# Optimization experiments

Measured on AMD Instinct MI355X. Metric: run time of the kernel, lower is better.

Reference implementation:

```python
import jax, jax.numpy as jnp
import numpy as np

B, L, D, H = 2, 2048, 1024, 16
DPH = D // H  # 64
EPS = 1e-5


def setup_inputs() -> dict:
    rng = jax.random.key(0)
    ks = jax.random.split(rng, 16)
    init = lambda k, shape: (jax.random.normal(k, shape, dtype=jnp.float32) * 0.02)
    return {
        "key": jax.random.normal(ks[0], (B, L, D), dtype=jnp.float32),
        "value": jax.random.normal(ks[1], (B, L, D), dtype=jnp.float32),
        "query": jax.random.normal(ks[2], (B, L, D), dtype=jnp.float32),
        "Wq": init(ks[3], (D, D)), "bq": jnp.zeros((D,), jnp.float32),
        "Wk": init(ks[4], (D, D)), "bk": jnp.zeros((D,), jnp.float32),
        "Wv": init(ks[5], (D, D)), "bv": jnp.zeros((D,), jnp.float32),
        "Wo": init(ks[6], (D, D)), "bo": jnp.zeros((D,), jnp.float32),
        "gamma": jnp.ones((D,), jnp.float32),
        "beta": jnp.zeros((D,), jnp.float32),
    }


def reference(key, value, query, Wq, bq, Wk, bk, Wv, bv, Wo, bo, gamma, beta):
    residual_in = query
    # torch Linear: x @ W.T + b
    k = key @ Wk.T + bk
    v = value @ Wv.T + bv
    q = query @ Wq.T + bq
    # faithful to source: flat view into (B*H, L, DPH) WITHOUT head transpose
    k = k.reshape(B * H, L, DPH)
    v = v.reshape(B * H, L, DPH)
    q = q.reshape(B * H, L, DPH)
    # faithful quirky scale: (dim_per_head // num_heads) ** -0.5
    scale = (DPH // H) ** (-0.5)
    scores = jnp.einsum("bqd,bkd->bqk", q, k) * scale  # [B*H, L, L]
    attention = jax.nn.softmax(scores, axis=2)
    context = jnp.einsum("bqk,bkd->bqd", attention, v)  # [B*H, L, DPH]
    context = context.reshape(B, L, D)
    output = context @ Wo.T + bo
    x = residual_in + output
    mean = jnp.mean(x, axis=-1, keepdims=True)
    var = jnp.var(x, axis=-1, keepdims=True)
    output = (x - mean) * jax.lax.rsqrt(var + EPS) * gamma + beta
    return (output, attention)
```

## Files before the change

### kernel.cpp

```cpp
#include <hip/hip_runtime.h>
#include <cstddef>
#include <cstdint>

#define Lseq   2048
#define Dmodel 1024
#define NGRP   32
#define MROWS  4096
#define EPS_LN 1e-5f

typedef short  s16x8 __attribute__((ext_vector_type(8)));
typedef float  f32x4 __attribute__((ext_vector_type(4)));
typedef unsigned short ushort_t;

__device__ __forceinline__ ushort_t f2bf(float f) {
    union { float f; unsigned u; } v; v.f = f;
    unsigned r = v.u + 0x7FFFu + ((v.u >> 16) & 1u);
    return (ushort_t)(r >> 16);
}

__device__ __forceinline__ unsigned cvt_pk_bf16(float lo, float hi) {
    unsigned r;
    asm("v_cvt_pk_bf16_f32 %0, %1, %2" : "=v"(r) : "v"(lo), "v"(hi));
    return r;
}

__device__ __forceinline__ void gld16(const ushort_t* g, ushort_t* lds) {
    __builtin_amdgcn_global_load_lds(
        (const __attribute__((address_space(1))) unsigned int*)(uintptr_t)g,
        (__attribute__((address_space(3))) unsigned int*)(uintptr_t)lds,
        16, 0, 0);
}

__device__ __forceinline__ int xcd_chunk32(int f) {
    return (f & 7) * 4 + ((f >> 3) & 3);
}

struct CvtArgs {
    const float* src[7];
    ushort_t*    dst[7];
    int          n8[7];
};

__global__ __launch_bounds__(256) void cvt_bf16(CvtArgs a)
{
    const int ti = blockIdx.y;
    const float* __restrict__ s = a.src[ti];
    ushort_t* __restrict__    d = a.dst[ti];
    const int n8 = a.n8[ti];
    for (int i = blockIdx.x * 256 + threadIdx.x; i < n8; i += gridDim.x * 256) {
        float4 x0 = reinterpret_cast<const float4*>(s)[i * 2];
        float4 x1 = reinterpret_cast<const float4*>(s)[i * 2 + 1];
        s16x8 o;
        o[0]=f2bf(x0.x); o[1]=f2bf(x0.y); o[2]=f2bf(x0.z); o[3]=f2bf(x0.w);
        o[4]=f2bf(x1.x); o[5]=f2bf(x1.y); o[6]=f2bf(x1.z); o[7]=f2bf(x1.w);
        reinterpret_cast<s16x8*>(d)[i] = o;
    }
}

struct QkvArgs {
    const ushort_t* A[3];
    const ushort_t* W[3];
    const float*    bias[3];
    ushort_t*       out[3];
};

__global__ __launch_bounds__(256) void gemm_qkv(QkvArgs a)
{
    __shared__ ushort_t As[128 * 64];
    __shared__ ushort_t Bs[128 * 64];
    const int z  = blockIdx.z;
    const int f  = blockIdx.x;
    const int m0 = xcd_chunk32(f) * 128;
    const int n0 = (f >> 5) * 128;

    const ushort_t* __restrict__ A = a.A[z];
    const ushort_t* __restrict__ W = a.W[z];
    const float*    __restrict__ bias = a.bias[z];
    ushort_t*       __restrict__ outv = a.out[z];

    const int t  = threadIdx.x;
    const int w  = t >> 6;
    const int l  = t & 63;
    const int lr = l & 15;
    const int lg = l >> 4;
    const int wm = w >> 1, wn = w & 1;

    const ushort_t* gA = A + (size_t)(m0 + w * 32 + (l >> 3)) * 1024 + (l & 7) * 8;
    const ushort_t* gB = W + (size_t)(n0 + w * 32 + (l >> 3)) * 1024 + (l & 7) * 8;
    ushort_t* lA = &As[(w * 32) * 64];
    ushort_t* lB = &Bs[(w * 32) * 64];

    f32x4 acc[4][4] = {};

    for (int k0 = 0; k0 < 1024; k0 += 64) {
#pragma unroll
        for (int j = 0; j < 4; ++j) {
            gld16(gA + (size_t)j * 8 * 1024 + k0, lA + j * 8 * 64);
            gld16(gB + (size_t)j * 8 * 1024 + k0, lB + j * 8 * 64);
        }
        __syncthreads();

#pragma unroll
        for (int kk = 0; kk < 2; ++kk) {
            s16x8 af[4], bf[4];
#pragma unroll
            for (int mi = 0; mi < 4; ++mi)
                af[mi] = *reinterpret_cast<const s16x8*>(&As[(wm * 64 + mi * 16 + lr) * 64 + kk * 32 + lg * 8]);
#pragma unroll
            for (int ni = 0; ni < 4; ++ni)
                bf[ni] = *reinterpret_cast<const s16x8*>(&Bs[(wn * 64 + ni * 16 + lr) * 64 + kk * 32 + lg * 8]);
#pragma unroll
            for (int mi = 0; mi < 4; ++mi)
#pragma unroll
                for (int ni = 0; ni < 4; ++ni)
                    acc[mi][ni] = __builtin_amdgcn_mfma_f32_16x16x32_bf16(af[mi], bf[ni], acc[mi][ni], 0, 0, 0);
        }
        __syncthreads();
    }

#pragma unroll
    for (int mi = 0; mi < 4; ++mi)
#pragma unroll
        for (int ni = 0; ni < 4; ++ni)
#pragma unroll
            for (int r = 0; r < 4; ++r) {
                int row = m0 + wm * 64 + mi * 16 + lg * 4 + r;
                int col = n0 + wn * 64 + ni * 16 + lr;
                outv[(size_t)row * 1024 + col] = f2bf(acc[mi][ni][r] + bias[col]);
            }
}

__global__ __launch_bounds__(256) void gemm_o(
    const ushort_t* __restrict__ A, const ushort_t* __restrict__ W,
    const float* __restrict__ bias, const float* __restrict__ resid,
    float* __restrict__ out)
{
    __shared__ ushort_t As[64 * 64];
    __shared__ ushort_t Bs[128 * 64];

    const int f  = blockIdx.x;
    const int m0 = ((f & 7) * 8 + ((f >> 3) & 7)) * 64;
    const int n0 = (f >> 6) * 128;

    const int t  = threadIdx.x;
    const int w  = t >> 6;
    const int l  = t & 63;
    const int lr = l & 15;
    const int lg = l >> 4;
    const int wm = w >> 1, wn = w & 1;

    const ushort_t* gA = A + (size_t)(m0 + w * 16 + (l >> 3)) * 1024 + (l & 7) * 8;
    const ushort_t* gB = W + (size_t)(n0 + w * 32 + (l >> 3)) * 1024 + (l & 7) * 8;
    ushort_t* lA = &As[(w * 16) * 64];
    ushort_t* lB = &Bs[(w * 32) * 64];

    f32x4 acc[2][4] = {};

    for (int k0 = 0; k0 < 1024; k0 += 64) {
#pragma unroll
        for (int j = 0; j < 2; ++j)
            gld16(gA + (size_t)j * 8 * 1024 + k0, lA + j * 8 * 64);
#pragma unroll
        for (int j = 0; j < 4; ++j)
            gld16(gB + (size_t)j * 8 * 1024 + k0, lB + j * 8 * 64);
        __syncthreads();

#pragma unroll
        for (int kk = 0; kk < 2; ++kk) {
            s16x8 af[2], bf[4];
#pragma unroll
            for (int mi = 0; mi < 2; ++mi)
                af[mi] = *reinterpret_cast<const s16x8*>(&As[(wm * 32 + mi * 16 + lr) * 64 + kk * 32 + lg * 8]);
#pragma unroll
            for (int ni = 0; ni < 4; ++ni)
                bf[ni] = *reinterpret_cast<const s16x8*>(&Bs[(wn * 64 + ni * 16 + lr) * 64 + kk * 32 + lg * 8]);
#pragma unroll
            for (int mi = 0; mi < 2; ++mi)
#pragma unroll
                for (int ni = 0; ni < 4; ++ni)
                    acc[mi][ni] = __builtin_amdgcn_mfma_f32_16x16x32_bf16(af[mi], bf[ni], acc[mi][ni], 0, 0, 0);
        }
        __syncthreads();
    }

#pragma unroll
    for (int mi = 0; mi < 2; ++mi)
#pragma unroll
        for (int ni = 0; ni < 4; ++ni)
#pragma unroll
            for (int r = 0; r < 4; ++r) {
                int row = m0 + wm * 32 + mi * 16 + lg * 4 + r;
                int col = n0 + wn * 64 + ni * 16 + lr;
                float v = acc[mi][ni][r] + bias[col] + resid[(size_t)row * 1024 + col];
                out[(size_t)row * 1024 + col] = v;
            }
}

__global__ __launch_bounds__(256) void transpose_v(
    const ushort_t* __restrict__ vb, ushort_t* __restrict__ vt)
{
    __shared__ ushort_t tile[64][72];
    const int g  = blockIdx.x;
    const int lt = blockIdx.y;
    const int t  = threadIdx.x;
#pragma unroll
    for (int it = 0; it < 2; ++it) {
        int s = t * 2 + it, row = s >> 3, sub = (s & 7) * 8;
        *reinterpret_cast<s16x8*>(&tile[row][sub]) =
            *reinterpret_cast<const s16x8*>(vb + ((size_t)(g*2048 + lt*64 + row))*64 + sub);
    }
    __syncthreads();
#pragma unroll
    for (int it = 0; it < 2; ++it) {
        int s = t * 2 + it, drow = s >> 3, sub = (s & 7) * 8;
        s16x8 o;
#pragma unroll
        for (int j = 0; j < 8; ++j) o[j] = (short)tile[sub + j][drow];
        *reinterpret_cast<s16x8*>(vt + ((size_t)(g*64 + drow))*2048 + lt*64 + sub) = o;
    }
}

__global__ __launch_bounds__(256) void attn_stats(
    const ushort_t* __restrict__ qb, const ushort_t* __restrict__ kb,
    float* __restrict__ invb)
{
    __shared__ ushort_t Ks[2][64][72];

    const int f  = blockIdx.x;
    const int g  = xcd_chunk32(f);
    const int r0 = (f >> 5) * 128;
    const int t  = threadIdx.x;
    const int w  = t >> 6;
    const int l  = t & 63;
    const int lr = l & 15;
    const int lg = l >> 4;
    const int srow0 = (t*2)   >> 3, ssub0 = ((t*2)   & 7) * 8;
    const int srow1 = (t*2+1) >> 3, ssub1 = ((t*2+1) & 7) * 8;

    s16x8 qf[2][2];
#pragma unroll
    for (int rf = 0; rf < 2; ++rf) {
        const ushort_t* qrow = qb + ((size_t)(g*2048 + r0 + w*32 + rf*16 + lr)) * 64;
        qf[rf][0] = *reinterpret_cast<const s16x8*>(qrow + lg*8);
        qf[rf][1] = *reinterpret_cast<const s16x8*>(qrow + 32 + lg*8);
    }

    *reinterpret_cast<s16x8*>(&Ks[0][srow0][ssub0]) =
        *reinterpret_cast<const s16x8*>(kb + ((size_t)(g*2048 + srow0))*64 + ssub0);
    *reinterpret_cast<s16x8*>(&Ks[0][srow1][ssub1]) =
        *reinterpret_cast<const s16x8*>(kb + ((size_t)(g*2048 + srow1))*64 + ssub1);
    __syncthreads();

    float lsum[2][4] = {};
    int cur = 0;

    for (int jc = 0; jc < 32; ++jc) {
        s16x8 nk0, nk1;
        if (jc < 31) {
            nk0 = *reinterpret_cast<const s16x8*>(kb + ((size_t)(g*2048 + (jc+1)*64 + srow0))*64 + ssub0);
            nk1 = *reinterpret_cast<const s16x8*>(kb + ((size_t)(g*2048 + (jc+1)*64 + srow1))*64 + ssub1);
        }
#pragma unroll
        for (int jf = 0; jf < 4; ++jf) {
            s16x8 b0 = *reinterpret_cast<const s16x8*>(&Ks[cur][jf*16 + lr][lg*8]);
            s16x8 b1 = *reinterpret_cast<const s16x8*>(&Ks[cur][jf*16 + lr][32 + lg*8]);
#pragma unroll
            for (int rf = 0; rf < 2; ++rf) {
                f32x4 sv = {};
                sv = __builtin_amdgcn_mfma_f32_16x16x32_bf16(qf[rf][0], b0, sv, 0, 0, 0);
                sv = __builtin_amdgcn_mfma_f32_16x16x32_bf16(qf[rf][1], b1, sv, 0, 0, 0);
#pragma unroll
                for (int r = 0; r < 4; ++r)
                    lsum[rf][r] += __expf(sv[r] * 0.5f);
            }
        }
        if (jc < 31) {
            *reinterpret_cast<s16x8*>(&Ks[cur^1][srow0][ssub0]) = nk0;
            *reinterpret_cast<s16x8*>(&Ks[cur^1][srow1][ssub1]) = nk1;
        }
        __syncthreads();
        cur ^= 1;
    }

#pragma unroll
    for (int rf = 0; rf < 2; ++rf)
#pragma unroll
        for (int r = 0; r < 4; ++r) {
            float v = lsum[rf][r];
            v += __shfl_xor(v, 1); v += __shfl_xor(v, 2);
            v += __shfl_xor(v, 4); v += __shfl_xor(v, 8);
            if (lr == 0)
                invb[(size_t)g*2048 + r0 + w*32 + rf*16 + lg*4 + r] = 1.f / v;
        }
}

__global__ __launch_bounds__(256) void attn_main(
    const ushort_t* __restrict__ qb, const ushort_t* __restrict__ kb,
    const ushort_t* __restrict__ vt, const float* __restrict__ invb,
    float* __restrict__ attn, ushort_t* __restrict__ ctxb)
{
    __shared__ ushort_t Ks[2][64][72];
    __shared__ ushort_t Vs[2][64][72];
    __shared__ ushort_t Ps[64][72];

    const int f  = blockIdx.x;
    const int g  = xcd_chunk32(f);
    const int r0 = (f >> 5) * 64;
    const int t  = threadIdx.x;
    const int w  = t >> 6;
    const int l  = t & 63;
    const int lr = l & 15;
    const int lg = l >> 4;
    const int srow0 = (t*2)   >> 3, ssub0 = ((t*2)   & 7) * 8;
    const int srow1 = (t*2+1) >> 3, ssub1 = ((t*2+1) & 7) * 8;

    s16x8 qf0, qf1;
    {
        const ushort_t* qrow = qb + ((size_t)(g*2048 + r0 + w*16 + lr)) * 64;
        qf0 = *reinterpret_cast<const s16x8*>(qrow + lg*8);
        qf1 = *reinterpret_cast<const s16x8*>(qrow + 32 + lg*8);
    }

    const float inv_s = invb[(size_t)g*2048 + r0 + w*16 + lr];
    float* arow = attn + (size_t)g*Lseq*Lseq + (size_t)(r0 + w*16 + lr)*Lseq + lg*4;

    *reinterpret_cast<s16x8*>(&Ks[0][srow0][ssub0]) =
        *reinterpret_cast<const s16x8*>(kb + ((size_t)(g*2048 + srow0))*64 + ssub0);
    *reinterpret_cast<s16x8*>(&Ks[0][srow1][ssub1]) =
        *reinterpret_cast<const s16x8*>(kb + ((size_t)(g*2048 + srow1))*64 + ssub1);
    *reinterpret_cast<s16x8*>(&Vs[0][srow0][ssub0]) =
        *reinterpret_cast<const s16x8*>(vt + ((size_t)(g*64 + srow0))*2048 + ssub0);
    *reinterpret_cast<s16x8*>(&Vs[0][srow1][ssub1]) =
        *reinterpret_cast<const s16x8*>(vt + ((size_t)(g*64 + srow1))*2048 + ssub1);
    __syncthreads();

    f32x4 ctx[4] = {};
    int cur = 0;

    for (int jc = 0; jc < 32; ++jc) {
        s16x8 nk0, nk1, nv0, nv1;
        if (jc < 31) {
            nk0 = *reinterpret_cast<const s16x8*>(kb + ((size_t)(g*2048 + (jc+1)*64 + srow0))*64 + ssub0);
            nk1 = *reinterpret_cast<const s16x8*>(kb + ((size_t)(g*2048 + (jc+1)*64 + srow1))*64 + ssub1);
            nv0 = *reinterpret_cast<const s16x8*>(vt + ((size_t)(g*64 + srow0))*2048 + (jc+1)*64 + ssub0);
            nv1 = *reinterpret_cast<const s16x8*>(vt + ((size_t)(g*64 + srow1))*2048 + (jc+1)*64 + ssub1);
        }

#pragma unroll
        for (int jf = 0; jf < 4; ++jf) {
            s16x8 a0 = *reinterpret_cast<const s16x8*>(&Ks[cur][jf*16 + lr][lg*8]);
            s16x8 a1 = *reinterpret_cast<const s16x8*>(&Ks[cur][jf*16 + lr][32 + lg*8]);
            f32x4 s = {};
            s = __builtin_amdgcn_mfma_f32_16x16x32_bf16(a0, qf0, s, 0, 0, 0);
            s = __builtin_amdgcn_mfma_f32_16x16x32_bf16(a1, qf1, s, 0, 0, 0);

            float e0 = __expf(s[0] * 0.5f);
            float e1 = __expf(s[1] * 0.5f);
            float e2 = __expf(s[2] * 0.5f);
            float e3 = __expf(s[3] * 0.5f);

            f32x4 o;
            o[0] = e0 * inv_s; o[1] = e1 * inv_s; o[2] = e2 * inv_s; o[3] = e3 * inv_s;
            *reinterpret_cast<f32x4*>(arow + jc*64 + jf*16) = o;

            unsigned p01 = cvt_pk_bf16(e0, e1);
            unsigned p23 = cvt_pk_bf16(e2, e3);
            uint2 pk; pk.x = p01; pk.y = p23;
            *reinterpret_cast<uint2*>(&Ps[w*16 + lr][jf*16 + lg*4]) = pk;
        }

#pragma unroll
        for (int kk = 0; kk < 2; ++kk) {
            s16x8 pa = *reinterpret_cast<const s16x8*>(&Ps[w*16 + lr][kk*32 + lg*8]);
#pragma unroll
            for (int ni = 0; ni < 4; ++ni) {
                s16x8 bv = *reinterpret_cast<const s16x8*>(&Vs[cur][ni*16 + lr][kk*32 + lg*8]);
                ctx[ni] = __builtin_amdgcn_mfma_f32_16x16x32_bf16(pa, bv, ctx[ni], 0, 0, 0);
            }
        }

        if (jc < 31) {
            *reinterpret_cast<s16x8*>(&Ks[cur^1][srow0][ssub0]) = nk0;
            *reinterpret_cast<s16x8*>(&Ks[cur^1][srow1][ssub1]) = nk1;
            *reinterpret_cast<s16x8*>(&Vs[cur^1][srow0][ssub0]) = nv0;
            *reinterpret_cast<s16x8*>(&Vs[cur^1][srow1][ssub1]) = nv1;
        }
        __syncthreads();
        cur ^= 1;
    }

#pragma unroll
    for (int ni = 0; ni < 4; ++ni)
#pragma unroll
        for (int r = 0; r < 4; ++r) {
            int l2 = r0 + w*16 + lg*4 + r;
            int d2 = ni*16 + lr;
            float iv = invb[(size_t)g*2048 + l2];
            ctxb[(size_t)g*Lseq*64 + (size_t)l2*64 + d2] = f2bf(ctx[ni][r] * iv);
        }
}

__global__ __launch_bounds__(256) void ln_kernel(
    float* __restrict__ x, const float* __restrict__ gamma,
    const float* __restrict__ beta, float* __restrict__ out)
{
    const int row = blockIdx.x;
    const int t   = threadIdx.x;
    const int c   = t * 4;

    float4 v = *reinterpret_cast<const float4*>(x + (size_t)row * Dmodel + c);
    float s  = v.x + v.y + v.z + v.w;
    float s2 = v.x*v.x + v.y*v.y + v.z*v.z + v.w*v.w;
    for (int off = 1; off < 64; off <<= 1) {
        s  += __shfl_xor(s, off);
        s2 += __shfl_xor(s2, off);
    }
    __shared__ float ssum[4], ssum2[4];
    int wid = t >> 6;
    if ((t & 63) == 0) { ssum[wid] = s; ssum2[wid] = s2; }
    __syncthreads();
    s  = ssum[0] + ssum[1] + ssum[2] + ssum[3];
    s2 = ssum2[0] + ssum2[1] + ssum2[2] + ssum2[3];

    float mean = s * (1.f / Dmodel);
    float var  = s2 * (1.f / Dmodel) - mean * mean;
    float rstd = rsqrtf(var + EPS_LN);

    float4 gv = *reinterpret_cast<const float4*>(gamma + c);
    float4 bv = *reinterpret_cast<const float4*>(beta + c);
    float4 o;
    o.x = (v.x - mean) * rstd * gv.x + bv.x;
    o.y = (v.y - mean) * rstd * gv.y + bv.y;
    o.z = (v.z - mean) * rstd * gv.z + bv.z;
    o.w = (v.w - mean) * rstd * gv.w + bv.w;
    *reinterpret_cast<float4*>(out + (size_t)row * Dmodel + c) = o;
}

extern "C" void kernel_launch(void* const* d_in, const int* in_sizes, int n_in,
                              void* d_out, int out_size, void* d_ws, size_t ws_size,
                              hipStream_t stream)
{
    const float* key   = (const float*)d_in[0];
    const float* value = (const float*)d_in[1];
    const float* query = (const float*)d_in[2];
    const float* Wq    = (const float*)d_in[3];
    const float* bq    = (const float*)d_in[4];
    const float* Wk    = (const float*)d_in[5];
    const float* bk    = (const float*)d_in[6];
    const float* Wv    = (const float*)d_in[7];
    const float* bv    = (const float*)d_in[8];
    const float* Wo    = (const float*)d_in[9];
    const float* bo    = (const float*)d_in[10];
    const float* gamma = (const float*)d_in[11];
    const float* beta  = (const float*)d_in[12];

    float* out  = (float*)d_out;
    float* attn = out + (size_t)MROWS * Dmodel;

    const size_t M1 = 1024 * 1024;
    ushort_t* ws   = (ushort_t*)d_ws;
    ushort_t* qb   = ws;
    ushort_t* kb   = ws + 4  * M1;
    ushort_t* vb   = ws + 8  * M1;
    ushort_t* vt   = ws + 12 * M1;
    ushort_t* qx   = ws + 16 * M1;
    ushort_t* kx   = ws + 20 * M1;
    ushort_t* vx   = ws + 24 * M1;
    ushort_t* wqx  = ws + 28 * M1;
    ushort_t* wkx  = ws + 29 * M1;
    ushort_t* wvx  = ws + 30 * M1;
    ushort_t* wox  = ws + 31 * M1;
    ushort_t* ctxb = qx;
    float*    invb = (float*)kx;

    CvtArgs ca;
    ca.src[0]=query; ca.dst[0]=qx;  ca.n8[0]=(int)(4*M1/8);
    ca.src[1]=key;   ca.dst[1]=kx;  ca.n8[1]=(int)(4*M1/8);
    ca.src[2]=value; ca.dst[2]=vx;  ca.n8[2]=(int)(4*M1/8);
    ca.src[3]=Wq;    ca.dst[3]=wqx; ca.n8[3]=(int)(M1/8);
    ca.src[4]=Wk;    ca.dst[4]=wkx; ca.n8[4]=(int)(M1/8);
    ca.src[5]=Wv;    ca.dst[5]=wvx; ca.n8[5]=(int)(M1/8);
    ca.src[6]=Wo;    ca.dst[6]=wox; ca.n8[6]=(int)(M1/8);
    cvt_bf16<<<dim3(512, 7), 256, 0, stream>>>(ca);

    QkvArgs qa;
    qa.A[0]=qx; qa.W[0]=wqx; qa.bias[0]=bq; qa.out[0]=qb;
    qa.A[1]=kx; qa.W[1]=wkx; qa.bias[1]=bk; qa.out[1]=kb;
    qa.A[2]=vx; qa.W[2]=wvx; qa.bias[2]=bv; qa.out[2]=vb;
    gemm_qkv<<<dim3(256, 1, 3), 256, 0, stream>>>(qa);

    transpose_v<<<dim3(NGRP, Lseq/64), 256, 0, stream>>>(vb, vt);

    attn_stats<<<dim3(512), 256, 0, stream>>>(qb, kb, invb);

    attn_main<<<dim3(1024), 256, 0, stream>>>(qb, kb, vt, invb, attn, ctxb);

    gemm_o<<<dim3(512), 256, 0, stream>>>(ctxb, wox, bo, query, out);

    ln_kernel<<<dim3(MROWS), 256, 0, stream>>>(out, gamma, beta, out);
}
```

Measured before the change: 298.5 us.

## Fuse softmax row-sum pass into attention kernel and keep P in registers

Removes the separate attn_stats launch and computes the row sums of exp(scores) inside attn_main as a first pass over K, storing the reciprocals in shared memory. The P tile is no longer staged through LDS. Instead, the V transpose permutes key order so each lane's packed bf16 exp values directly form the MFMA A operand. LDS padding also changes. The first pass now runs at the 64-row tile granularity rather than 128, so the QK^T work for the stats is done with less reuse, in exchange for one fewer launch and less LDS traffic.

Result: faster. 278.9 us, median of 2 (-6.6%).

```diff
diff --git a/kernel.cpp b/kernel.cpp
--- a/kernel.cpp
+++ b/kernel.cpp
@@ -33,6 +33,10 @@
 
 __device__ __forceinline__ int xcd_chunk32(int f) {
     return (f & 7) * 4 + ((f >> 3) & 3);
+}
+
+__device__ __forceinline__ int perm64(int s) {
+    return (s & 32) + ((s & 4) << 2) + (((s >> 3) & 3) << 2) + (s & 3);
 }
 
 struct CvtArgs {
@@ -215,93 +219,22 @@
         int s = t * 2 + it, drow = s >> 3, sub = (s & 7) * 8;
         s16x8 o;
 #pragma unroll
-        for (int j = 0; j < 8; ++j) o[j] = (short)tile[sub + j][drow];
+        for (int j = 0; j < 8; ++j) {
+            int key = perm64(sub + j);
+            o[j] = (short)tile[key][drow];
+        }
         *reinterpret_cast<s16x8*>(vt + ((size_t)(g*64 + drow))*2048 + lt*64 + sub) = o;
     }
-}
-
-__global__ __launch_bounds__(256) void attn_stats(
-    const ushort_t* __restrict__ qb, const ushort_t* __restrict__ kb,
-    float* __restrict__ invb)
-{
-    __shared__ ushort_t Ks[2][64][72];
-
-    const int f  = blockIdx.x;
-    const int g  = xcd_chunk32(f);
-    const int r0 = (f >> 5) * 128;
-    const int t  = threadIdx.x;
-    const int w  = t >> 6;
-    const int l  = t & 63;
-    const int lr = l & 15;
-    const int lg = l >> 4;
-    const int srow0 = (t*2)   >> 3, ssub0 = ((t*2)   & 7) * 8;
-    const int srow1 = (t*2+1) >> 3, ssub1 = ((t*2+1) & 7) * 8;
-
-    s16x8 qf[2][2];
-#pragma unroll
-    for (int rf = 0; rf < 2; ++rf) {
-        const ushort_t* qrow = qb + ((size_t)(g*2048 + r0 + w*32 + rf*16 + lr)) * 64;
-        qf[rf][0] = *reinterpret_cast<const s16x8*>(qrow + lg*8);
-        qf[rf][1] = *reinterpret_cast<const s16x8*>(qrow + 32 + lg*8);
-    }
-
-    *reinterpret_cast<s16x8*>(&Ks[0][srow0][ssub0]) =
-        *reinterpret_cast<const s16x8*>(kb + ((size_t)(g*2048 + srow0))*64 + ssub0);
-    *reinterpret_cast<s16x8*>(&Ks[0][srow1][ssub1]) =
-        *reinterpret_cast<const s16x8*>(kb + ((size_t)(g*2048 + srow1))*64 + ssub1);
-    __syncthreads();
-
-    float lsum[2][4] = {};
-    int cur = 0;
-
-    for (int jc = 0; jc < 32; ++jc) {
-        s16x8 nk0, nk1;
-        if (jc < 31) {
-            nk0 = *reinterpret_cast<const s16x8*>(kb + ((size_t)(g*2048 + (jc+1)*64 + srow0))*64 + ssub0);
-            nk1 = *reinterpret_cast<const s16x8*>(kb + ((size_t)(g*2048 + (jc+1)*64 + srow1))*64 + ssub1);
-        }
-#pragma unroll
-        for (int jf = 0; jf < 4; ++jf) {
-            s16x8 b0 = *reinterpret_cast<const s16x8*>(&Ks[cur][jf*16 + lr][lg*8]);
-            s16x8 b1 = *reinterpret_cast<const s16x8*>(&Ks[cur][jf*16 + lr][32 + lg*8]);
-#pragma unroll
-            for (int rf = 0; rf < 2; ++rf) {
-                f32x4 sv = {};
-                sv = __builtin_amdgcn_mfma_f32_16x16x32_bf16(qf[rf][0], b0, sv, 0, 0, 0);
-                sv = __builtin_amdgcn_mfma_f32_16x16x32_bf16(qf[rf][1], b1, sv, 0, 0, 0);
-#pragma unroll
-                for (int r = 0; r < 4; ++r)
-                    lsum[rf][r] += __expf(sv[r] * 0.5f);
-            }
-        }
-        if (jc < 31) {
-            *reinterpret_cast<s16x8*>(&Ks[cur^1][srow0][ssub0]) = nk0;
-            *reinterpret_cast<s16x8*>(&Ks[cur^1][srow1][ssub1]) = nk1;
-        }
-        __syncthreads();
-        cur ^= 1;
-    }
-
-#pragma unroll
-    for (int rf = 0; rf < 2; ++rf)
-#pragma unroll
-        for (int r = 0; r < 4; ++r) {
-            float v = lsum[rf][r];
-            v += __shfl_xor(v, 1); v += __shfl_xor(v, 2);
-            v += __shfl_xor(v, 4); v += __shfl_xor(v, 8);
-            if (lr == 0)
-                invb[(size_t)g*2048 + r0 + w*32 + rf*16 + lg*4 + r] = 1.f / v;
-        }
 }
 
 __global__ __launch_bounds__(256) void attn_main(
     const ushort_t* __restrict__ qb, const ushort_t* __restrict__ kb,
-    const ushort_t* __restrict__ vt, const float* __restrict__ invb,
+    const ushort_t* __restrict__ vt,
     float* __restrict__ attn, ushort_t* __restrict__ ctxb)
 {
-    __shared__ ushort_t Ks[2][64][72];
-    __shared__ ushort_t Vs[2][64][72];
-    __shared__ ushort_t Ps[64][72];
+    __shared__ ushort_t Ks[2][64][88];
+    __shared__ ushort_t Vs[2][64][88];
+    __shared__ float    wsum[4][16];
 
     const int f  = blockIdx.x;
     const int g  = xcd_chunk32(f);
@@ -321,7 +254,49 @@
         qf1 = *reinterpret_cast<const s16x8*>(qrow + 32 + lg*8);
     }
 
-    const float inv_s = invb[(size_t)g*2048 + r0 + w*16 + lr];
+    *reinterpret_cast<s16x8*>(&Ks[0][srow0][ssub0]) =
+        *reinterpret_cast<const s16x8*>(kb + ((size_t)(g*2048 + srow0))*64 + ssub0);
+    *reinterpret_cast<s16x8*>(&Ks[0][srow1][ssub1]) =
+        *reinterpret_cast<const s16x8*>(kb + ((size_t)(g*2048 + srow1))*64 + ssub1);
+    __syncthreads();
+
+    float lsum[4] = {0.f, 0.f, 0.f, 0.f};
+    int cur = 0;
+
+    for (int jc = 0; jc < 32; ++jc) {
+        s16x8 nk0, nk1;
+        if (jc < 31) {
+            nk0 = *reinterpret_cast<const s16x8*>(kb + ((size_t)(g*2048 + (jc+1)*64 + srow0))*64 + ssub0);
+            nk1 = *reinterpret_cast<const s16x8*>(kb + ((size_t)(g*2048 + (jc+1)*64 + srow1))*64 + ssub1);
+        }
+#pragma unroll
+        for (int jf = 0; jf < 4; ++jf) {
+            s16x8 b0 = *reinterpret_cast<const s16x8*>(&Ks[cur][jf*16 + lr][lg*8]);
+            s16x8 b1 = *reinterpret_cast<const s16x8*>(&Ks[cur][jf*16 + lr][32 + lg*8]);
+            f32x4 sv = {};
+            sv = __builtin_amdgcn_mfma_f32_16x16x32_bf16(qf0, b0, sv, 0, 0, 0);
+            sv = __builtin_amdgcn_mfma_f32_16x16x32_bf16(qf1, b1, sv, 0, 0, 0);
+#pragma unroll
+            for (int r = 0; r < 4; ++r)
+                lsum[r] += __expf(sv[r] * 0.5f);
+        }
+        if (jc < 31) {
+            *reinterpret_cast<s16x8*>(&Ks[cur^1][srow0][ssub0]) = nk0;
+            *reinterpret_cast<s16x8*>(&Ks[cur^1][srow1][ssub1]) = nk1;
+        }
+        __syncthreads();
+        cur ^= 1;
+    }
+#pragma unroll
+    for (int r = 0; r < 4; ++r) {
+        float v = lsum[r];
+        v += __shfl_xor(v, 1); v += __shfl_xor(v, 2);
+        v += __shfl_xor(v, 4); v += __shfl_xor(v, 8);
+        if (lr == 0) wsum[w][lg*4 + r] = 1.f / v;
+    }
+    __syncthreads();
+
+    const float inv_s = wsum[w][lr];
     float* arow = attn + (size_t)g*Lseq*Lseq + (size_t)(r0 + w*16 + lr)*Lseq + lg*4;
 
     *reinterpret_cast<s16x8*>(&Ks[0][srow0][ssub0]) =
@@ -335,7 +310,7 @@
     __syncthreads();
 
     f32x4 ctx[4] = {};
-    int cur = 0;
+    cur = 0;
 
     for (int jc = 0; jc < 32; ++jc) {
         s16x8 nk0, nk1, nv0, nv1;
@@ -346,6 +321,7 @@
             nv1 = *reinterpret_cast<const s16x8*>(vt + ((size_t)(g*64 + srow1))*2048 + (jc+1)*64 + ssub1);
         }
 
+        uint2 pj[4];
 #pragma unroll
         for (int jf = 0; jf < 4; ++jf) {
             s16x8 a0 = *reinterpret_cast<const s16x8*>(&Ks[cur][jf*16 + lr][lg*8]);
@@ -363,19 +339,19 @@
             o[0] = e0 * inv_s; o[1] = e1 * inv_s; o[2] = e2 * inv_s; o[3] = e3 * inv_s;
             *reinterpret_cast<f32x4*>(arow + jc*64 + jf*16) = o;
 
-            unsigned p01 = cvt_pk_bf16(e0, e1);
-            unsigned p23 = cvt_pk_bf16(e2, e3);
-            uint2 pk; pk.x = p01; pk.y = p23;
-            *reinterpret_cast<uint2*>(&Ps[w*16 + lr][jf*16 + lg*4]) = pk;
+            pj[jf].x = cvt_pk_bf16(e0, e1);
+            pj[jf].y = cvt_pk_bf16(e2, e3);
         }
 
 #pragma unroll
         for (int kk = 0; kk < 2; ++kk) {
-            s16x8 pa = *reinterpret_cast<const s16x8*>(&Ps[w*16 + lr][kk*32 + lg*8]);
+            union { s16x8 v; uint2 u[2]; } pu;
+            pu.u[0] = pj[2*kk];
+            pu.u[1] = pj[2*kk + 1];
 #pragma unroll
             for (int ni = 0; ni < 4; ++ni) {
                 s16x8 bv = *reinterpret_cast<const s16x8*>(&Vs[cur][ni*16 + lr][kk*32 + lg*8]);
-                ctx[ni] = __builtin_amdgcn_mfma_f32_16x16x32_bf16(pa, bv, ctx[ni], 0, 0, 0);
+                ctx[ni] = __builtin_amdgcn_mfma_f32_16x16x32_bf16(pu.v, bv, ctx[ni], 0, 0, 0);
             }
         }
 
@@ -395,7 +371,7 @@
         for (int r = 0; r < 4; ++r) {
             int l2 = r0 + w*16 + lg*4 + r;
             int d2 = ni*16 + lr;
-            float iv = invb[(size_t)g*2048 + l2];
+            float iv = wsum[w][lg*4 + r];
             ctxb[(size_t)g*Lseq*64 + (size_t)l2*64 + d2] = f2bf(ctx[ni][r] * iv);
         }
 }
@@ -471,7 +447,6 @@
     ushort_t* wvx  = ws + 30 * M1;
     ushort_t* wox  = ws + 31 * M1;
     ushort_t* ctxb = qx;
-    float*    invb = (float*)kx;
 
     CvtArgs ca;
     ca.src[0]=query; ca.dst[0]=qx;  ca.n8[0]=(int)(4*M1/8);
@@ -491,9 +466,7 @@
 
     transpose_v<<<dim3(NGRP, Lseq/64), 256, 0, stream>>>(vb, vt);
 
-    attn_stats<<<dim3(512), 256, 0, stream>>>(qb, kb, invb);
-
-    attn_main<<<dim3(1024), 256, 0, stream>>>(qb, kb, vt, invb, attn, ctxb);
+    attn_main<<<dim3(1024), 256, 0, stream>>>(qb, kb, vt, attn, ctxb);
 
     gemm_o<<<dim3(512), 256, 0, stream>>>(ctxb, wox, bo, query, out);
 
```
